# Kernel tuning notes

Measured on AMD Instinct MI355X. Metric: run time of the kernel, lower is better.

## Reference

```python
import math
import jax, jax.numpy as jnp
import numpy as np

B, L, D_MODEL = 2, 2048, 1024
N_HEAD, HEAD_DIM = 16, 64
ATT_SCALE = 1.0  # divisor is sqrt(head_dim ** attention_scale)


def setup_inputs() -> dict:
    key = jax.random.key(0)
    ks = jax.random.split(key, 6)
    HD = N_HEAD * HEAD_DIM
    # Xavier-uniform style init for projection weights (stored as [in, out])
    def xavier(k, fan_in, fan_out):
        lim = math.sqrt(6.0 / (fan_in + fan_out))
        return jax.random.uniform(k, (fan_in, fan_out), jnp.float32, -lim, lim)
    return {
        "x":  jax.random.normal(ks[0], (B, L, D_MODEL), jnp.float32),
        "Wq": xavier(ks[1], D_MODEL, HD), "bq": jnp.zeros((HD,), jnp.float32),
        "Wk": xavier(ks[2], D_MODEL, HD), "bk": jnp.zeros((HD,), jnp.float32),
        "Wv": xavier(ks[3], D_MODEL, HD), "bv": jnp.zeros((HD,), jnp.float32),
        "Wo": xavier(ks[4], HD, D_MODEL),
        "bo": jax.random.uniform(ks[5], (D_MODEL,), jnp.float32, -1.0 / math.sqrt(HD), 1.0 / math.sqrt(HD)),
    }


def reference(x, Wq, bq, Wk, bk, Wv, bv, Wo, bo):
    b, l, _ = x.shape
    # QKV projections -> [B, L, H, Dh]
    q = (x @ Wq + bq).reshape(b, l, N_HEAD, HEAD_DIM)
    k = (x @ Wk + bk).reshape(b, l, N_HEAD, HEAD_DIM)
    v = (x @ Wv + bv).reshape(b, l, N_HEAD, HEAD_DIM)
    scale = 1.0 / math.sqrt(HEAD_DIM ** ATT_SCALE)
    # Unnormalized (no softmax) attention: (Q K^T / sqrt(Dh)) V
    scores = jnp.einsum("blhd,bmhd->bhlm", q, k) * scale  # [B,H,L,L]
    attn = jnp.einsum("bhlm,bmhd->blhd", scores, v)        # [B,L,H,Dh]
    out = attn.reshape(b, l, N_HEAD * HEAD_DIM) @ Wo + bo  # dispatcher
    return out
```

## Files before the change

kernel.cpp:

```cpp
#include <hip/hip_runtime.h>
#include <stdint.h>

#define B_ 2
#define L_ 2048
#define DM 1024
#define NH 16
#define DH 64
#define M_ (B_*L_)
#define NQKV 3072

typedef short short8 __attribute__((ext_vector_type(8)));
typedef float f32x4 __attribute__((ext_vector_type(4)));

__device__ __forceinline__ unsigned short f2b(float f) {
    union { float f; unsigned int u; } v; v.f = f;
    unsigned int u = v.u;
    return (unsigned short)((u + 0x7fffu + ((u >> 16) & 1u)) >> 16);
}

__device__ __forceinline__ void gld_lds16(const void* g, void* l) {
    __builtin_amdgcn_global_load_lds(
        (const __attribute__((address_space(1))) void*)g,
        (__attribute__((address_space(3))) void*)l, 16, 0, 0);
}

__global__ __launch_bounds__(256)
void setup_kernel(const float* __restrict__ x,
                  const float* __restrict__ Wq, const float* __restrict__ Wk,
                  const float* __restrict__ Wv, const float* __restrict__ Wo,
                  const float* __restrict__ bq, const float* __restrict__ bk,
                  const float* __restrict__ bv,
                  unsigned short* __restrict__ xb, unsigned short* __restrict__ WqkvT,
                  unsigned short* __restrict__ WoT, float* __restrict__ biasq,
                  float* __restrict__ KtV)
{
    __shared__ float tile[32][33];
    const int bid = blockIdx.x;
    const int t = threadIdx.x;

    if (bid < 2048) {
        int i = (bid * 256 + t) * 8;
        float4 a0 = *(const float4*)(x + i);
        float4 a1 = *(const float4*)(x + i + 4);
        uint4 p;
        p.x = (unsigned)f2b(a0.x) | ((unsigned)f2b(a0.y) << 16);
        p.y = (unsigned)f2b(a0.z) | ((unsigned)f2b(a0.w) << 16);
        p.z = (unsigned)f2b(a1.x) | ((unsigned)f2b(a1.y) << 16);
        p.w = (unsigned)f2b(a1.z) | ((unsigned)f2b(a1.w) << 16);
        *(uint4*)(xb + i) = p;
    } else if (bid < 2048 + 4096) {
        int wb = bid - 2048;
        int wi = wb >> 10;
        int tid = wb & 1023;
        const float* W = (wi == 0) ? Wq : (wi == 1) ? Wk : (wi == 2) ? Wv : Wo;
        float s = (wi == 1) ? 0.125f : 1.0f;
        int n0 = (tid & 31) * 32, k0 = (tid >> 5) * 32;
        int r = t >> 3, c4 = (t & 7) << 2;
        float4 v = *(const float4*)(W + (size_t)(k0 + r) * DM + n0 + c4);
        tile[r][c4+0] = v.x; tile[r][c4+1] = v.y; tile[r][c4+2] = v.z; tile[r][c4+3] = v.w;
        __syncthreads();
        uint2 o;
        o.x = (unsigned)f2b(tile[c4+0][r]*s) | ((unsigned)f2b(tile[c4+1][r]*s) << 16);
        o.y = (unsigned)f2b(tile[c4+2][r]*s) | ((unsigned)f2b(tile[c4+3][r]*s) << 16);
        int f = n0 + r;
        size_t drow;
        unsigned short* dst;
        if (wi == 0)      { dst = WqkvT; drow = f; }
        else if (wi == 1) { dst = WqkvT; drow = 1024 + (f >> 6) * 128 + (f & 63); }
        else if (wi == 2) { dst = WqkvT; drow = 1024 + (f >> 6) * 128 + 64 + (f & 63); }
        else              { dst = WoT;   drow = f; }
        *(uint2*)(dst + drow * DM + k0 + c4) = o;
    } else if (bid < 2048 + 4096 + 12) {
        int n = (bid - 6144) * 256 + t;
        float v;
        if (n < 1024) v = bq[n];
        else {
            int kv = (n - 1024) >> 7, r = (n - 1024) & 127;
            v = (r < 64) ? 0.125f * bk[kv * 64 + r] : bv[kv * 64 + (r - 64)];
        }
        biasq[n] = v;
    } else {
        int i = ((bid - 6156) * 256 + t) * 4;
        float4 z; z.x = z.y = z.z = z.w = 0.f;
        *(float4*)(KtV + i) = z;
    }
}

__global__ __launch_bounds__(256)
void qkv_fused_kernel(const unsigned short* __restrict__ A,
                      const unsigned short* __restrict__ Bt,
                      const float* __restrict__ biasq,
                      unsigned short* __restrict__ Qb,
                      float* __restrict__ KtV)
{
    __shared__ __align__(16) char smem[34816];
    unsigned short* As = (unsigned short*)smem;
    unsigned short* Bs = (unsigned short*)(smem + 8192);

    const int bid = blockIdx.x;
    const int xcd = bid & 7, local = bid >> 3;
    const int mt = xcd * 4 + (local & 3);
    const int nt = local >> 2;
    const int m0 = mt * 128, n0 = nt * 128;

    const int t = threadIdx.x;
    const int w = t >> 6, lane = t & 63;
    const int quad = lane >> 4, l16 = lane & 15;
    const int wm = w >> 1, wn = w & 1;

    f32x4 acc[4][4];
    #pragma unroll
    for (int i = 0; i < 4; i++)
        #pragma unroll
        for (int j = 0; j < 4; j++)
            #pragma unroll
            for (int r = 0; r < 4; r++) acc[i][j][r] = 0.f;

    const int srow = t >> 2;
    const int schunk = t & 3;

    for (int kk = 0; kk < DM; kk += 32) {
        #pragma unroll
        for (int p = 0; p < 2; p++) {
            int row = p * 64 + srow;
            int g = schunk ^ ((row >> 1) & 3);
            gld_lds16(A  + (size_t)(m0 + row) * DM + kk + g * 8,
                      (char*)As + p * 4096 + w * 1024);
            gld_lds16(Bt + (size_t)(n0 + row) * DM + kk + g * 8,
                      (char*)Bs + p * 4096 + w * 1024);
        }
        __syncthreads();

        short8 afr[4], bfr[4];
        #pragma unroll
        for (int i = 0; i < 4; i++) {
            int am = wm * 64 + i * 16 + l16;
            afr[i] = *(const short8*)((const char*)As + am * 64 + ((quad ^ ((am >> 1) & 3)) << 4));
            int bn = wn * 64 + i * 16 + l16;
            bfr[i] = *(const short8*)((const char*)Bs + bn * 64 + ((quad ^ ((bn >> 1) & 3)) << 4));
        }
        #pragma unroll
        for (int i = 0; i < 4; i++)
            #pragma unroll
            for (int j = 0; j < 4; j++)
                acc[i][j] = __builtin_amdgcn_mfma_f32_16x16x32_bf16(afr[i], bfr[j], acc[i][j], 0, 0, 0);
        __syncthreads();
    }

    #pragma unroll
    for (int j = 0; j < 4; j++) {
        float bv = biasq[n0 + wn * 64 + j * 16 + l16];
        #pragma unroll
        for (int i = 0; i < 4; i++)
            #pragma unroll
            for (int r = 0; r < 4; r++) acc[i][j][r] += bv;
    }

    if (nt < 8) {
        #pragma unroll
        for (int j = 0; j < 4; j++) {
            int col = n0 + wn * 64 + j * 16 + l16;
            #pragma unroll
            for (int i = 0; i < 4; i++) {
                #pragma unroll
                for (int r = 0; r < 4; r++) {
                    int row = m0 + wm * 64 + i * 16 + quad * 4 + r;
                    Qb[(size_t)row * DM + col] = f2b(acc[i][j][r]);
                }
            }
        }
        return;
    }

    const int h  = nt - 8;
    const int bh = (m0 >> 11) * NH + h;
    unsigned short (*Xt)[136] = (unsigned short (*)[136])smem;

    #pragma unroll
    for (int j = 0; j < 4; j++) {
        int c = wn * 64 + j * 16 + l16;
        #pragma unroll
        for (int i = 0; i < 4; i++) {
            int l0 = wm * 64 + i * 16 + quad * 4;
            uint2 o;
            o.x = (unsigned)f2b(acc[i][j][0]) | ((unsigned)f2b(acc[i][j][1]) << 16);
            o.y = (unsigned)f2b(acc[i][j][2]) | ((unsigned)f2b(acc[i][j][3]) << 16);
            *(uint2*)&Xt[c][l0] = o;
        }
    }
    __syncthreads();

    f32x4 kacc[4];
    #pragma unroll
    for (int j = 0; j < 4; j++)
        #pragma unroll
        for (int r = 0; r < 4; r++) kacc[j][r] = 0.f;

    #pragma unroll
    for (int ks = 0; ks < 4; ks++) {
        short8 af = *(const short8*)&Xt[w * 16 + l16][ks * 32 + quad * 8];
        #pragma unroll
        for (int j = 0; j < 4; j++) {
            short8 bfr = *(const short8*)&Xt[64 + j * 16 + l16][ks * 32 + quad * 8];
            kacc[j] = __builtin_amdgcn_mfma_f32_16x16x32_bf16(af, bfr, kacc[j], 0, 0, 0);
        }
    }

    float* dst = KtV + (size_t)bh * 64 * 64;
    #pragma unroll
    for (int j = 0; j < 4; j++) {
        int col = j * 16 + l16;
        #pragma unroll
        for (int r = 0; r < 4; r++) {
            int row = w * 16 + quad * 4 + r;
            atomicAdd(dst + row * 64 + col, kacc[j][r]);
        }
    }
}

__global__ __launch_bounds__(256)
void zmat_kernel(const unsigned short* __restrict__ WoT, const float* __restrict__ KtV,
                 unsigned short* __restrict__ ZT)
{
    __shared__ __align__(16) unsigned short Asl[64][72];
    __shared__ __align__(16) unsigned short Bsl[64][72];

    const int bh = blockIdx.x, nt0 = blockIdx.y;
    const int b = bh >> 4, h = bh & 15;
    const int t = threadIdx.x;
    const int wave = t >> 6, lane = t & 63;
    const int quad = lane >> 4, l16 = lane & 15;
    const int n0 = nt0 * 64;
    const int row = t >> 2, c0 = (t & 3) << 4;

    const unsigned short* ap = WoT + (size_t)(n0 + row) * DM + h * DH + c0;
    *(uint4*)&Asl[row][c0]     = *(const uint4*)ap;
    *(uint4*)&Asl[row][c0 + 8] = *(const uint4*)(ap + 8);

    const float* kp = KtV + ((size_t)bh * 64 + row) * 64 + c0;
    #pragma unroll
    for (int j = 0; j < 16; j++) Bsl[row][c0 + j] = f2b(kp[j]);
    __syncthreads();

    f32x4 acc[4];
    #pragma unroll
    for (int i = 0; i < 4; i++)
        #pragma unroll
        for (int r = 0; r < 4; r++) acc[i][r] = 0.f;

    #pragma unroll
    for (int ks = 0; ks < 2; ks++) {
        short8 af = *(const short8*)&Asl[wave * 16 + l16][ks * 32 + quad * 8];
        #pragma unroll
        for (int nt = 0; nt < 4; nt++) {
            short8 bfr = *(const short8*)&Bsl[nt * 16 + l16][ks * 32 + quad * 8];
            acc[nt] = __builtin_amdgcn_mfma_f32_16x16x32_bf16(af, bfr, acc[nt], 0, 0, 0);
        }
    }

    unsigned short* zb = ZT + (size_t)b * 1024 * 1024 + (size_t)h * DH;
    #pragma unroll
    for (int nt = 0; nt < 4; nt++) {
        int col = nt * 16 + l16;
        #pragma unroll
        for (int r = 0; r < 4; r++) {
            int zr = n0 + wave * 16 + quad * 4 + r;
            zb[(size_t)zr * 1024 + col] = f2b(acc[nt][r]);
        }
    }
}

__global__ __launch_bounds__(256)
void out_gemm_kernel(const unsigned short* __restrict__ A,
                     const unsigned short* __restrict__ Bt,
                     const float* __restrict__ bias,
                     float* __restrict__ C)
{
    __shared__ __align__(16) unsigned short As[128 * 64];
    __shared__ __align__(16) unsigned short Bs[64 * 64];

    const int bid = blockIdx.x;
    const int xcd = bid & 7, local = bid >> 3;
    const int mt = xcd * 4 + (local & 3);
    const int nt = local >> 2;
    const int m0 = mt * 128, n0 = nt * 64;

    const int t = threadIdx.x;
    const int w = t >> 6, lane = t & 63;
    const int quad = lane >> 4, l16 = lane & 15;

    const unsigned short* Btb = Bt + (size_t)(m0 >> 11) * 1024 * 1024;

    f32x4 acc[2][4];
    #pragma unroll
    for (int i = 0; i < 2; i++)
        #pragma unroll
        for (int j = 0; j < 4; j++)
            #pragma unroll
            for (int r = 0; r < 4; r++) acc[i][j][r] = 0.f;

    for (int kk = 0; kk < DM; kk += 64) {
        #pragma unroll
        for (int p = 0; p < 4; p++) {
            int c = p * 256 + t;
            int row = c >> 3, slot = c & 7;
            int g = slot ^ ((row >> 1) & 7);
            gld_lds16(A + (size_t)(m0 + row) * DM + kk + g * 8,
                      (char*)As + p * 4096 + w * 1024);
        }
        #pragma unroll
        for (int p = 0; p < 2; p++) {
            int c = p * 256 + t;
            int row = c >> 3, slot = c & 7;
            int g = slot ^ ((row >> 1) & 7);
            gld_lds16(Btb + (size_t)(n0 + row) * DM + kk + g * 8,
                      (char*)Bs + p * 4096 + w * 1024);
        }
        __syncthreads();

        #pragma unroll
        for (int ks = 0; ks < 2; ks++) {
            int kc = ks * 4 + quad;
            short8 afr[2], bfr[4];
            #pragma unroll
            for (int i = 0; i < 2; i++) {
                int am = w * 32 + i * 16 + l16;
                afr[i] = *(const short8*)((const char*)As + am * 128 + ((kc ^ ((am >> 1) & 7)) << 4));
            }
            #pragma unroll
            for (int j = 0; j < 4; j++) {
                int bn = j * 16 + l16;
                bfr[j] = *(const short8*)((const char*)Bs + bn * 128 + ((kc ^ ((bn >> 1) & 7)) << 4));
            }
            #pragma unroll
            for (int i = 0; i < 2; i++)
                #pragma unroll
                for (int j = 0; j < 4; j++)
                    acc[i][j] = __builtin_amdgcn_mfma_f32_16x16x32_bf16(afr[i], bfr[j], acc[i][j], 0, 0, 0);
        }
        __syncthreads();
    }

    #pragma unroll
    for (int j = 0; j < 4; j++) {
        int col = n0 + j * 16 + l16;
        float bv = bias[col];
        #pragma unroll
        for (int i = 0; i < 2; i++) {
            #pragma unroll
            for (int r = 0; r < 4; r++) {
                int row = m0 + w * 32 + i * 16 + quad * 4 + r;
                C[(size_t)row * DM + col] = acc[i][j][r] + bv;
            }
        }
    }
}


extern "C" void kernel_launch(void* const* d_in, const int* in_sizes, int n_in,
                              void* d_out, int out_size, void* d_ws, size_t ws_size,
                              hipStream_t stream)
{
    const float* x  = (const float*)d_in[0];
    const float* Wq = (const float*)d_in[1];
    const float* bq = (const float*)d_in[2];
    const float* Wk = (const float*)d_in[3];
    const float* bk = (const float*)d_in[4];
    const float* Wv = (const float*)d_in[5];
    const float* bv = (const float*)d_in[6];
    const float* Wo = (const float*)d_in[7];
    const float* bo = (const float*)d_in[8];

    char* ws = (char*)d_ws;
    unsigned short* xb    = (unsigned short*)(ws);
    unsigned short* WqkvT = (unsigned short*)(ws + (size_t)8  * 1024 * 1024);
    unsigned short* WoT   = (unsigned short*)(ws + (size_t)14 * 1024 * 1024);
    float*          biasq = (float*)         (ws + (size_t)16 * 1024 * 1024);
    unsigned short* Qb    = (unsigned short*)(ws + (size_t)17 * 1024 * 1024);
    unsigned short* ZT    = (unsigned short*)(ws + (size_t)25 * 1024 * 1024);
    float*          KtV   = (float*)         (ws + (size_t)29 * 1024 * 1024);

    setup_kernel<<<6284, 256, 0, stream>>>(x, Wq, Wk, Wv, Wo, bq, bk, bv,
                                           xb, WqkvT, WoT, biasq, KtV);

    qkv_fused_kernel<<<768, 256, 0, stream>>>(xb, WqkvT, biasq, Qb, KtV);

    zmat_kernel<<<dim3(B_ * NH, 16), 256, 0, stream>>>(WoT, KtV, ZT);

    out_gemm_kernel<<<512, 256, 0, stream>>>(Qb, ZT, bo, (float*)d_out);
}
```

Baseline: 143.3 us.

## Fold Q projection and Wo into per-batch combined weight matrix

Instead of computing Q = xWq and then Q·Z, precompute per batch P = [Wq;bq]·KtV per head and M = Wo^T·P^T, so the output is x·M plus a bias row folded in via an augmented row. This removes the Q GEMM (a third of the QKV projection) and the Qb write/read, replacing it with two smaller weight-sized GEMMs per batch. It adds an extra kernel launch and an extra bf16 rounding of the combined matrix, which changes numerics slightly.

Result: slower. 155.1 us (+8.2%).

```diff
diff --git a/kernel.cpp b/kernel.cpp
--- a/kernel.cpp
+++ b/kernel.cpp
@@ -7,7 +7,7 @@
 #define NH 16
 #define DH 64
 #define M_ (B_*L_)
-#define NQKV 3072
+#define KP 1152
 
 typedef short short8 __attribute__((ext_vector_type(8)));
 typedef float f32x4 __attribute__((ext_vector_type(4)));
@@ -16,6 +16,11 @@
     union { float f; unsigned int u; } v; v.f = f;
     unsigned int u = v.u;
     return (unsigned short)((u + 0x7fffu + ((u >> 16) & 1u)) >> 16);
+}
+
+__device__ __forceinline__ float b2f(unsigned short b) {
+    union { float f; unsigned int u; } v; v.u = ((unsigned)b) << 16;
+    return v.f;
 }
 
 __device__ __forceinline__ void gld_lds16(const void* g, void* l) {
@@ -30,9 +35,9 @@
                   const float* __restrict__ Wv, const float* __restrict__ Wo,
                   const float* __restrict__ bq, const float* __restrict__ bk,
                   const float* __restrict__ bv,
-                  unsigned short* __restrict__ xb, unsigned short* __restrict__ WqkvT,
-                  unsigned short* __restrict__ WoT, float* __restrict__ biasq,
-                  float* __restrict__ KtV)
+                  unsigned short* __restrict__ xb, unsigned short* __restrict__ WkvT,
+                  unsigned short* __restrict__ WoT, unsigned short* __restrict__ WqA,
+                  float* __restrict__ biaskv, float* __restrict__ KtV)
 {
     __shared__ float tile[32][33];
     const int bid = blockIdx.x;
@@ -48,12 +53,12 @@
         p.z = (unsigned)f2b(a1.x) | ((unsigned)f2b(a1.y) << 16);
         p.w = (unsigned)f2b(a1.z) | ((unsigned)f2b(a1.w) << 16);
         *(uint4*)(xb + i) = p;
-    } else if (bid < 2048 + 4096) {
+    } else if (bid < 2048 + 3072) {
         int wb = bid - 2048;
         int wi = wb >> 10;
         int tid = wb & 1023;
-        const float* W = (wi == 0) ? Wq : (wi == 1) ? Wk : (wi == 2) ? Wv : Wo;
-        float s = (wi == 1) ? 0.125f : 1.0f;
+        const float* W = (wi == 0) ? Wk : (wi == 1) ? Wv : Wo;
+        float s = (wi == 0) ? 0.125f : 1.0f;
         int n0 = (tid & 31) * 32, k0 = (tid >> 5) * 32;
         int r = t >> 3, c4 = (t & 7) << 2;
         float4 v = *(const float4*)(W + (size_t)(k0 + r) * DM + n0 + c4);
@@ -65,33 +70,66 @@
         int f = n0 + r;
         size_t drow;
         unsigned short* dst;
-        if (wi == 0)      { dst = WqkvT; drow = f; }
-        else if (wi == 1) { dst = WqkvT; drow = 1024 + (f >> 6) * 128 + (f & 63); }
-        else if (wi == 2) { dst = WqkvT; drow = 1024 + (f >> 6) * 128 + 64 + (f & 63); }
-        else              { dst = WoT;   drow = f; }
+        if (wi == 0)      { dst = WkvT; drow = (f >> 6) * 128 + (f & 63); }
+        else if (wi == 1) { dst = WkvT; drow = (f >> 6) * 128 + 64 + (f & 63); }
+        else              { dst = WoT;  drow = f; }
         *(uint2*)(dst + drow * DM + k0 + c4) = o;
-    } else if (bid < 2048 + 4096 + 12) {
-        int n = (bid - 6144) * 256 + t;
-        float v;
-        if (n < 1024) v = bq[n];
-        else {
-            int kv = (n - 1024) >> 7, r = (n - 1024) & 127;
-            v = (r < 64) ? 0.125f * bk[kv * 64 + r] : bv[kv * 64 + (r - 64)];
-        }
-        biasq[n] = v;
+    } else if (bid < 2048 + 3072 + 512) {
+        int i = ((bid - 5120) * 256 + t) * 8;
+        float4 a0 = *(const float4*)(Wq + i);
+        float4 a1 = *(const float4*)(Wq + i + 4);
+        uint4 p;
+        p.x = (unsigned)f2b(a0.x) | ((unsigned)f2b(a0.y) << 16);
+        p.y = (unsigned)f2b(a0.z) | ((unsigned)f2b(a0.w) << 16);
+        p.z = (unsigned)f2b(a1.x) | ((unsigned)f2b(a1.y) << 16);
+        p.w = (unsigned)f2b(a1.z) | ((unsigned)f2b(a1.w) << 16);
+        *(uint4*)(WqA + i) = p;
+    } else if (bid < 2048 + 3072 + 512 + 64) {
+        int idx = ((bid - 5632) * 256 + t) * 8;
+        uint4 p;
+        if (idx < 1024) {
+            float4 a0 = *(const float4*)(bq + idx);
+            float4 a1 = *(const float4*)(bq + idx + 4);
+            p.x = (unsigned)f2b(a0.x) | ((unsigned)f2b(a0.y) << 16);
+            p.y = (unsigned)f2b(a0.z) | ((unsigned)f2b(a0.w) << 16);
+            p.z = (unsigned)f2b(a1.x) | ((unsigned)f2b(a1.y) << 16);
+            p.w = (unsigned)f2b(a1.z) | ((unsigned)f2b(a1.w) << 16);
+        } else {
+            p.x = p.y = p.z = p.w = 0u;
+        }
+        *(uint4*)(WqA + 1024 * 1024 + idx) = p;
+    } else if (bid < 2048 + 3072 + 512 + 64 + 2) {
+        int i = ((bid - 5696) * 256 + t) * 4;
+        float o0, o1, o2, o3;
+        {
+            int n = i + 0, kv = n >> 7, rr = n & 127;
+            o0 = (rr < 64) ? 0.125f * bk[kv * 64 + rr] : bv[kv * 64 + (rr - 64)];
+        }
+        {
+            int n = i + 1, kv = n >> 7, rr = n & 127;
+            o1 = (rr < 64) ? 0.125f * bk[kv * 64 + rr] : bv[kv * 64 + (rr - 64)];
+        }
+        {
+            int n = i + 2, kv = n >> 7, rr = n & 127;
+            o2 = (rr < 64) ? 0.125f * bk[kv * 64 + rr] : bv[kv * 64 + (rr - 64)];
+        }
+        {
+            int n = i + 3, kv = n >> 7, rr = n & 127;
+            o3 = (rr < 64) ? 0.125f * bk[kv * 64 + rr] : bv[kv * 64 + (rr - 64)];
+        }
+        *(float4*)(biaskv + i) = make_float4(o0, o1, o2, o3);
     } else {
-        int i = ((bid - 6156) * 256 + t) * 4;
+        int i = ((bid - 5698) * 256 + t) * 4;
         float4 z; z.x = z.y = z.z = z.w = 0.f;
         *(float4*)(KtV + i) = z;
     }
 }
 
 __global__ __launch_bounds__(256)
-void qkv_fused_kernel(const unsigned short* __restrict__ A,
-                      const unsigned short* __restrict__ Bt,
-                      const float* __restrict__ biasq,
-                      unsigned short* __restrict__ Qb,
-                      float* __restrict__ KtV)
+void kv_fused_kernel(const unsigned short* __restrict__ A,
+                     const unsigned short* __restrict__ Bt,
+                     const float* __restrict__ biaskv,
+                     float* __restrict__ KtV)
 {
     __shared__ __align__(16) char smem[34816];
     unsigned short* As = (unsigned short*)smem;
@@ -149,30 +187,14 @@
 
     #pragma unroll
     for (int j = 0; j < 4; j++) {
-        float bv = biasq[n0 + wn * 64 + j * 16 + l16];
+        float bvv = biaskv[n0 + wn * 64 + j * 16 + l16];
         #pragma unroll
         for (int i = 0; i < 4; i++)
             #pragma unroll
-            for (int r = 0; r < 4; r++) acc[i][j][r] += bv;
-    }
-
-    if (nt < 8) {
-        #pragma unroll
-        for (int j = 0; j < 4; j++) {
-            int col = n0 + wn * 64 + j * 16 + l16;
-            #pragma unroll
-            for (int i = 0; i < 4; i++) {
-                #pragma unroll
-                for (int r = 0; r < 4; r++) {
-                    int row = m0 + wm * 64 + i * 16 + quad * 4 + r;
-                    Qb[(size_t)row * DM + col] = f2b(acc[i][j][r]);
-                }
-            }
-        }
-        return;
-    }
-
-    const int h  = nt - 8;
+            for (int r = 0; r < 4; r++) acc[i][j][r] += bvv;
+    }
+
+    const int h  = nt;
     const int bh = (m0 >> 11) * NH + h;
     unsigned short (*Xt)[136] = (unsigned short (*)[136])smem;
 
@@ -219,54 +241,155 @@
 }
 
 __global__ __launch_bounds__(256)
-void zmat_kernel(const unsigned short* __restrict__ WoT, const float* __restrict__ KtV,
-                 unsigned short* __restrict__ ZT)
+void pmat_kernel(const unsigned short* __restrict__ WqA, const float* __restrict__ KtV,
+                 unsigned short* __restrict__ P)
 {
-    __shared__ __align__(16) unsigned short Asl[64][72];
-    __shared__ __align__(16) unsigned short Bsl[64][72];
-
-    const int bh = blockIdx.x, nt0 = blockIdx.y;
+    __shared__ __align__(16) unsigned short As[128 * 64];
+    __shared__ __align__(16) unsigned short Bs[64][72];
+
+    const int bh = blockIdx.x;
+    const int rt = blockIdx.y;
     const int b = bh >> 4, h = bh & 15;
     const int t = threadIdx.x;
-    const int wave = t >> 6, lane = t & 63;
+    const int w = t >> 6, lane = t & 63;
     const int quad = lane >> 4, l16 = lane & 15;
-    const int n0 = nt0 * 64;
-    const int row = t >> 2, c0 = (t & 3) << 4;
-
-    const unsigned short* ap = WoT + (size_t)(n0 + row) * DM + h * DH + c0;
-    *(uint4*)&Asl[row][c0]     = *(const uint4*)ap;
-    *(uint4*)&Asl[row][c0 + 8] = *(const uint4*)(ap + 8);
-
-    const float* kp = KtV + ((size_t)bh * 64 + row) * 64 + c0;
-    #pragma unroll
-    for (int j = 0; j < 16; j++) Bsl[row][c0 + j] = f2b(kp[j]);
+
+    #pragma unroll
+    for (int p = 0; p < 4; p++) {
+        int c = p * 256 + t;
+        int row = c >> 3, slot = c & 7;
+        int g = slot ^ ((row >> 1) & 7);
+        gld_lds16(WqA + (size_t)(rt * 128 + row) * DM + h * 64 + g * 8,
+                  (char*)As + p * 4096 + w * 1024);
+    }
+    {
+        const int d1 = t >> 2, c0 = (t & 3) * 16;
+        const float* kp = KtV + (size_t)bh * 64 * 64 + d1 * 64 + c0;
+        #pragma unroll
+        for (int j = 0; j < 16; j++)
+            Bs[c0 + j][d1] = f2b(kp[j]);
+    }
     __syncthreads();
 
-    f32x4 acc[4];
-    #pragma unroll
-    for (int i = 0; i < 4; i++)
-        #pragma unroll
-        for (int r = 0; r < 4; r++) acc[i][r] = 0.f;
+    f32x4 acc[2][4];
+    #pragma unroll
+    for (int i = 0; i < 2; i++)
+        #pragma unroll
+        for (int j = 0; j < 4; j++)
+            #pragma unroll
+            for (int r = 0; r < 4; r++) acc[i][j][r] = 0.f;
 
     #pragma unroll
     for (int ks = 0; ks < 2; ks++) {
-        short8 af = *(const short8*)&Asl[wave * 16 + l16][ks * 32 + quad * 8];
-        #pragma unroll
-        for (int nt = 0; nt < 4; nt++) {
-            short8 bfr = *(const short8*)&Bsl[nt * 16 + l16][ks * 32 + quad * 8];
-            acc[nt] = __builtin_amdgcn_mfma_f32_16x16x32_bf16(af, bfr, acc[nt], 0, 0, 0);
-        }
-    }
-
-    unsigned short* zb = ZT + (size_t)b * 1024 * 1024 + (size_t)h * DH;
-    #pragma unroll
-    for (int nt = 0; nt < 4; nt++) {
-        int col = nt * 16 + l16;
-        #pragma unroll
-        for (int r = 0; r < 4; r++) {
-            int zr = n0 + wave * 16 + quad * 4 + r;
-            zb[(size_t)zr * 1024 + col] = f2b(acc[nt][r]);
-        }
+        int kc = ks * 4 + quad;
+        short8 afr[2], bfr[4];
+        #pragma unroll
+        for (int i = 0; i < 2; i++) {
+            int am = w * 32 + i * 16 + l16;
+            afr[i] = *(const short8*)((const char*)As + am * 128 + ((kc ^ ((am >> 1) & 7)) << 4));
+        }
+        #pragma unroll
+        for (int j = 0; j < 4; j++)
+            bfr[j] = *(const short8*)&Bs[j * 16 + l16][ks * 32 + quad * 8];
+        #pragma unroll
+        for (int i = 0; i < 2; i++)
+            #pragma unroll
+            for (int j = 0; j < 4; j++)
+                acc[i][j] = __builtin_amdgcn_mfma_f32_16x16x32_bf16(afr[i], bfr[j], acc[i][j], 0, 0, 0);
+    }
+
+    unsigned short* pb = P + ((size_t)b * KP + rt * 128) * DM + h * 64;
+    #pragma unroll
+    for (int j = 0; j < 4; j++) {
+        int col = j * 16 + l16;
+        #pragma unroll
+        for (int i = 0; i < 2; i++)
+            #pragma unroll
+            for (int rr = 0; rr < 4; rr++) {
+                int row = w * 32 + i * 16 + quad * 4 + rr;
+                pb[(size_t)row * DM + col] = f2b(acc[i][j][rr]);
+            }
+    }
+}
+
+__global__ __launch_bounds__(256)
+void mmat_kernel(const unsigned short* __restrict__ WoT, const unsigned short* __restrict__ P,
+                 unsigned short* __restrict__ MT)
+{
+    __shared__ __align__(16) unsigned short As[128 * 64];
+    __shared__ __align__(16) unsigned short Bs[64 * 64];
+
+    const int bid = blockIdx.x;
+    const int bb = bid / 144;
+    const int r144 = bid % 144;
+    const int mt = r144 & 7, nt = r144 >> 3;
+    const int m0 = mt * 128, n0 = nt * 64;
+
+    const int t = threadIdx.x;
+    const int w = t >> 6, lane = t & 63;
+    const int quad = lane >> 4, l16 = lane & 15;
+
+    f32x4 acc[2][4];
+    #pragma unroll
+    for (int i = 0; i < 2; i++)
+        #pragma unroll
+        for (int j = 0; j < 4; j++)
+            #pragma unroll
+            for (int r = 0; r < 4; r++) acc[i][j][r] = 0.f;
+
+    for (int kk = 0; kk < DM; kk += 64) {
+        #pragma unroll
+        for (int p = 0; p < 4; p++) {
+            int c = p * 256 + t;
+            int row = c >> 3, slot = c & 7;
+            int g = slot ^ ((row >> 1) & 7);
+            gld_lds16(WoT + (size_t)(m0 + row) * DM + kk + g * 8,
+                      (char*)As + p * 4096 + w * 1024);
+        }
+        #pragma unroll
+        for (int p = 0; p < 2; p++) {
+            int c = p * 256 + t;
+            int row = c >> 3, slot = c & 7;
+            int g = slot ^ ((row >> 1) & 7);
+            gld_lds16(P + ((size_t)bb * KP + n0 + row) * DM + kk + g * 8,
+                      (char*)Bs + p * 4096 + w * 1024);
+        }
+        __syncthreads();
+
+        #pragma unroll
+        for (int ks = 0; ks < 2; ks++) {
+            int kc = ks * 4 + quad;
+            short8 afr[2], bfr[4];
+            #pragma unroll
+            for (int i = 0; i < 2; i++) {
+                int am = w * 32 + i * 16 + l16;
+                afr[i] = *(const short8*)((const char*)As + am * 128 + ((kc ^ ((am >> 1) & 7)) << 4));
+            }
+            #pragma unroll
+            for (int j = 0; j < 4; j++) {
+                int bn = j * 16 + l16;
+                bfr[j] = *(const short8*)((const char*)Bs + bn * 128 + ((kc ^ ((bn >> 1) & 7)) << 4));
+            }
+            #pragma unroll
+            for (int i = 0; i < 2; i++)
+                #pragma unroll
+                for (int j = 0; j < 4; j++)
+                    acc[i][j] = __builtin_amdgcn_mfma_f32_16x16x32_bf16(afr[i], bfr[j], acc[i][j], 0, 0, 0);
+        }
+        __syncthreads();
+    }
+
+    unsigned short* mb = MT + (size_t)bb * 1024 * KP;
+    #pragma unroll
+    for (int j = 0; j < 4; j++) {
+        int col = n0 + j * 16 + l16;
+        #pragma unroll
+        for (int i = 0; i < 2; i++)
+            #pragma unroll
+            for (int rr = 0; rr < 4; rr++) {
+                int row = m0 + w * 32 + i * 16 + quad * 4 + rr;
+                mb[(size_t)row * KP + col] = f2b(acc[i][j][rr]);
+            }
     }
 }
 
@@ -289,7 +412,7 @@
     const int w = t >> 6, lane = t & 63;
     const int quad = lane >> 4, l16 = lane & 15;
 
-    const unsigned short* Btb = Bt + (size_t)(m0 >> 11) * 1024 * 1024;
+    const unsigned short* Btb = Bt + (size_t)(m0 >> 11) * 1024 * KP;
 
     f32x4 acc[2][4];
     #pragma unroll
@@ -313,7 +436,7 @@
             int c = p * 256 + t;
             int row = c >> 3, slot = c & 7;
             int g = slot ^ ((row >> 1) & 7);
-            gld_lds16(Btb + (size_t)(n0 + row) * DM + kk + g * 8,
+            gld_lds16(Btb + (size_t)(n0 + row) * KP + kk + g * 8,
                       (char*)Bs + p * 4096 + w * 1024);
         }
         __syncthreads();
@@ -344,13 +467,13 @@
     #pragma unroll
     for (int j = 0; j < 4; j++) {
         int col = n0 + j * 16 + l16;
-        float bv = bias[col];
+        float bvv = bias[col] + b2f(Btb[(size_t)col * KP + 1024]);
         #pragma unroll
         for (int i = 0; i < 2; i++) {
             #pragma unroll
             for (int r = 0; r < 4; r++) {
                 int row = m0 + w * 32 + i * 16 + quad * 4 + r;
-                C[(size_t)row * DM + col] = acc[i][j][r] + bv;
+                C[(size_t)row * DM + col] = acc[i][j][r] + bvv;
             }
         }
     }
@@ -372,20 +495,23 @@
     const float* bo = (const float*)d_in[8];
 
     char* ws = (char*)d_ws;
-    unsigned short* xb    = (unsigned short*)(ws);
-    unsigned short* WqkvT = (unsigned short*)(ws + (size_t)8  * 1024 * 1024);
-    unsigned short* WoT   = (unsigned short*)(ws + (size_t)14 * 1024 * 1024);
-    float*          biasq = (float*)         (ws + (size_t)16 * 1024 * 1024);
-    unsigned short* Qb    = (unsigned short*)(ws + (size_t)17 * 1024 * 1024);
-    unsigned short* ZT    = (unsigned short*)(ws + (size_t)25 * 1024 * 1024);
-    float*          KtV   = (float*)         (ws + (size_t)29 * 1024 * 1024);
-
-    setup_kernel<<<6284, 256, 0, stream>>>(x, Wq, Wk, Wv, Wo, bq, bk, bv,
-                                           xb, WqkvT, WoT, biasq, KtV);
-
-    qkv_fused_kernel<<<768, 256, 0, stream>>>(xb, WqkvT, biasq, Qb, KtV);
-
-    zmat_kernel<<<dim3(B_ * NH, 16), 256, 0, stream>>>(WoT, KtV, ZT);
-
-    out_gemm_kernel<<<512, 256, 0, stream>>>(Qb, ZT, bo, (float*)d_out);
-}
+    unsigned short* xb     = (unsigned short*)(ws);
+    unsigned short* WkvT   = (unsigned short*)(ws + (size_t)8  * 1024 * 1024);
+    unsigned short* WoT    = (unsigned short*)(ws + (size_t)12 * 1024 * 1024);
+    unsigned short* WqA    = (unsigned short*)(ws + (size_t)14 * 1024 * 1024);
+    float*          biaskv = (float*)         (ws + (size_t)16 * 1024 * 1024 + 262144);
+    float*          KtV    = (float*)         (ws + (size_t)17 * 1024 * 1024);
+    unsigned short* P      = (unsigned short*)(ws + (size_t)18 * 1024 * 1024);
+    unsigned short* MT     = (unsigned short*)(ws + (size_t)23 * 1024 * 1024);
+
+    setup_kernel<<<5826, 256, 0, stream>>>(x, Wq, Wk, Wv, Wo, bq, bk, bv,
+                                           xb, WkvT, WoT, WqA, biaskv, KtV);
+
+    kv_fused_kernel<<<512, 256, 0, stream>>>(xb, WkvT, biaskv, KtV);
+
+    pmat_kernel<<<dim3(32, 9), 256, 0, stream>>>(WqA, KtV, P);
+
+    mmat_kernel<<<288, 256, 0, stream>>>(WoT, P, MT);
+
+    out_gemm_kernel<<<512, 256, 0, stream>>>(xb, MT, bo, (float*)d_out);
+}
```

## Deepen QKV GEMM K-step to 64 and enlarge output GEMM tile to 128x128

Applied to the files above, without the earlier changes.

The QKV GEMM now stages a 64-wide K slice per iteration instead of 32, using an 8-chunk XOR swizzle and two MFMA sub-steps per barrier pair. This halves the number of synchronisation rounds. The output GEMM moves from 128x64 to 128x128 tiles with a 2x2 wave layout and 16 accumulators per wave, which halves the grid to 256 blocks. The larger tiles improve data reuse per LDS load, at the cost of more LDS and registers per block and fewer blocks to fill the CUs.

Measured after the change: 158.2 us. +10.4%, slower.

```diff
diff --git a/kernel.cpp b/kernel.cpp
--- a/kernel.cpp
+++ b/kernel.cpp
@@ -95,7 +95,7 @@
 {
     __shared__ __align__(16) char smem[34816];
     unsigned short* As = (unsigned short*)smem;
-    unsigned short* Bs = (unsigned short*)(smem + 8192);
+    unsigned short* Bs = (unsigned short*)(smem + 16384);
 
     const int bid = blockIdx.x;
     const int xcd = bid & 7, local = bid >> 3;
@@ -116,34 +116,42 @@
             #pragma unroll
             for (int r = 0; r < 4; r++) acc[i][j][r] = 0.f;
 
-    const int srow = t >> 2;
-    const int schunk = t & 3;
-
-    for (int kk = 0; kk < DM; kk += 32) {
-        #pragma unroll
-        for (int p = 0; p < 2; p++) {
-            int row = p * 64 + srow;
-            int g = schunk ^ ((row >> 1) & 3);
-            gld_lds16(A  + (size_t)(m0 + row) * DM + kk + g * 8,
+    for (int kk = 0; kk < DM; kk += 64) {
+        #pragma unroll
+        for (int p = 0; p < 4; p++) {
+            int c = p * 256 + t;
+            int row = c >> 3, slot = c & 7;
+            int g = slot ^ ((row >> 1) & 7);
+            gld_lds16(A + (size_t)(m0 + row) * DM + kk + g * 8,
                       (char*)As + p * 4096 + w * 1024);
+        }
+        #pragma unroll
+        for (int p = 0; p < 4; p++) {
+            int c = p * 256 + t;
+            int row = c >> 3, slot = c & 7;
+            int g = slot ^ ((row >> 1) & 7);
             gld_lds16(Bt + (size_t)(n0 + row) * DM + kk + g * 8,
                       (char*)Bs + p * 4096 + w * 1024);
         }
         __syncthreads();
 
-        short8 afr[4], bfr[4];
-        #pragma unroll
-        for (int i = 0; i < 4; i++) {
-            int am = wm * 64 + i * 16 + l16;
-            afr[i] = *(const short8*)((const char*)As + am * 64 + ((quad ^ ((am >> 1) & 3)) << 4));
-            int bn = wn * 64 + i * 16 + l16;
-            bfr[i] = *(const short8*)((const char*)Bs + bn * 64 + ((quad ^ ((bn >> 1) & 3)) << 4));
-        }
-        #pragma unroll
-        for (int i = 0; i < 4; i++)
-            #pragma unroll
-            for (int j = 0; j < 4; j++)
-                acc[i][j] = __builtin_amdgcn_mfma_f32_16x16x32_bf16(afr[i], bfr[j], acc[i][j], 0, 0, 0);
+        #pragma unroll
+        for (int ks = 0; ks < 2; ks++) {
+            int kc = ks * 4 + quad;
+            short8 afr[4], bfr[4];
+            #pragma unroll
+            for (int i = 0; i < 4; i++) {
+                int am = wm * 64 + i * 16 + l16;
+                afr[i] = *(const short8*)((const char*)As + am * 128 + ((kc ^ ((am >> 1) & 7)) << 4));
+                int bn = wn * 64 + i * 16 + l16;
+                bfr[i] = *(const short8*)((const char*)Bs + bn * 128 + ((kc ^ ((bn >> 1) & 7)) << 4));
+            }
+            #pragma unroll
+            for (int i = 0; i < 4; i++)
+                #pragma unroll
+                for (int j = 0; j < 4; j++)
+                    acc[i][j] = __builtin_amdgcn_mfma_f32_16x16x32_bf16(afr[i], bfr[j], acc[i][j], 0, 0, 0);
+        }
         __syncthreads();
     }
 
@@ -277,23 +285,24 @@
                      float* __restrict__ C)
 {
     __shared__ __align__(16) unsigned short As[128 * 64];
-    __shared__ __align__(16) unsigned short Bs[64 * 64];
+    __shared__ __align__(16) unsigned short Bs[128 * 64];
 
     const int bid = blockIdx.x;
     const int xcd = bid & 7, local = bid >> 3;
     const int mt = xcd * 4 + (local & 3);
     const int nt = local >> 2;
-    const int m0 = mt * 128, n0 = nt * 64;
+    const int m0 = mt * 128, n0 = nt * 128;
 
     const int t = threadIdx.x;
     const int w = t >> 6, lane = t & 63;
     const int quad = lane >> 4, l16 = lane & 15;
+    const int wm = w >> 1, wn = w & 1;
 
     const unsigned short* Btb = Bt + (size_t)(m0 >> 11) * 1024 * 1024;
 
-    f32x4 acc[2][4];
-    #pragma unroll
-    for (int i = 0; i < 2; i++)
+    f32x4 acc[4][4];
+    #pragma unroll
+    for (int i = 0; i < 4; i++)
         #pragma unroll
         for (int j = 0; j < 4; j++)
             #pragma unroll
@@ -309,7 +318,7 @@
                       (char*)As + p * 4096 + w * 1024);
         }
         #pragma unroll
-        for (int p = 0; p < 2; p++) {
+        for (int p = 0; p < 4; p++) {
             int c = p * 256 + t;
             int row = c >> 3, slot = c & 7;
             int g = slot ^ ((row >> 1) & 7);
@@ -321,19 +330,16 @@
         #pragma unroll
         for (int ks = 0; ks < 2; ks++) {
             int kc = ks * 4 + quad;
-            short8 afr[2], bfr[4];
-            #pragma unroll
-            for (int i = 0; i < 2; i++) {
-                int am = w * 32 + i * 16 + l16;
+            short8 afr[4], bfr[4];
+            #pragma unroll
+            for (int i = 0; i < 4; i++) {
+                int am = wm * 64 + i * 16 + l16;
                 afr[i] = *(const short8*)((const char*)As + am * 128 + ((kc ^ ((am >> 1) & 7)) << 4));
+                int bn = wn * 64 + i * 16 + l16;
+                bfr[i] = *(const short8*)((const char*)Bs + bn * 128 + ((kc ^ ((bn >> 1) & 7)) << 4));
             }
             #pragma unroll
-            for (int j = 0; j < 4; j++) {
-                int bn = j * 16 + l16;
-                bfr[j] = *(const short8*)((const char*)Bs + bn * 128 + ((kc ^ ((bn >> 1) & 7)) << 4));
-            }
-            #pragma unroll
-            for (int i = 0; i < 2; i++)
+            for (int i = 0; i < 4; i++)
                 #pragma unroll
                 for (int j = 0; j < 4; j++)
                     acc[i][j] = __builtin_amdgcn_mfma_f32_16x16x32_bf16(afr[i], bfr[j], acc[i][j], 0, 0, 0);
@@ -343,13 +349,13 @@
 
     #pragma unroll
     for (int j = 0; j < 4; j++) {
-        int col = n0 + j * 16 + l16;
+        int col = n0 + wn * 64 + j * 16 + l16;
         float bv = bias[col];
         #pragma unroll
-        for (int i = 0; i < 2; i++) {
+        for (int i = 0; i < 4; i++) {
             #pragma unroll
             for (int r = 0; r < 4; r++) {
-                int row = m0 + w * 32 + i * 16 + quad * 4 + r;
+                int row = m0 + wm * 64 + i * 16 + quad * 4 + r;
                 C[(size_t)row * DM + col] = acc[i][j][r] + bv;
             }
         }
@@ -387,5 +393,5 @@
 
     zmat_kernel<<<dim3(B_ * NH, 16), 256, 0, stream>>>(WoT, KtV, ZT);
 
-    out_gemm_kernel<<<512, 256, 0, stream>>>(Qb, ZT, bo, (float*)d_out);
-}
+    out_gemm_kernel<<<256, 256, 0, stream>>>(Qb, ZT, bo, (float*)d_out);
+}
```

## Double-buffer LDS tiles in QKV and output GEMM main loops

Applied to the files above, without the earlier changes.

Both the fused QKV GEMM and the output projection GEMM now use two LDS buffers. The next k-tile's global-to-LDS loads are issued before the MFMA work on the current tile, leaving one barrier per iteration instead of two. The aim is to hide global load latency behind compute. The output GEMM's LDS footprint grows to 48KB, and an extra barrier is added before the QKV epilogue reuses shared memory, both of which may reduce occupancy.

Measured after the change: 150.6 us. 1.05x slower.

```diff
diff --git a/kernel.cpp b/kernel.cpp
--- a/kernel.cpp
+++ b/kernel.cpp
@@ -94,8 +94,6 @@
                       float* __restrict__ KtV)
 {
     __shared__ __align__(16) char smem[34816];
-    unsigned short* As = (unsigned short*)smem;
-    unsigned short* Bs = (unsigned short*)(smem + 8192);
 
     const int bid = blockIdx.x;
     const int xcd = bid & 7, local = bid >> 3;
@@ -119,33 +117,45 @@
     const int srow = t >> 2;
     const int schunk = t & 3;
 
-    for (int kk = 0; kk < DM; kk += 32) {
+    auto stage = [&](int buf, int kk) {
         #pragma unroll
         for (int p = 0; p < 2; p++) {
             int row = p * 64 + srow;
             int g = schunk ^ ((row >> 1) & 3);
             gld_lds16(A  + (size_t)(m0 + row) * DM + kk + g * 8,
-                      (char*)As + p * 4096 + w * 1024);
+                      smem + buf * 16384 + p * 4096 + w * 1024);
             gld_lds16(Bt + (size_t)(n0 + row) * DM + kk + g * 8,
-                      (char*)Bs + p * 4096 + w * 1024);
-        }
-        __syncthreads();
-
+                      smem + buf * 16384 + 8192 + p * 4096 + w * 1024);
+        }
+    };
+    auto compute = [&](int buf) {
+        const char* Asb = smem + buf * 16384;
+        const char* Bsb = Asb + 8192;
         short8 afr[4], bfr[4];
         #pragma unroll
         for (int i = 0; i < 4; i++) {
             int am = wm * 64 + i * 16 + l16;
-            afr[i] = *(const short8*)((const char*)As + am * 64 + ((quad ^ ((am >> 1) & 3)) << 4));
+            afr[i] = *(const short8*)(Asb + am * 64 + ((quad ^ ((am >> 1) & 3)) << 4));
             int bn = wn * 64 + i * 16 + l16;
-            bfr[i] = *(const short8*)((const char*)Bs + bn * 64 + ((quad ^ ((bn >> 1) & 3)) << 4));
+            bfr[i] = *(const short8*)(Bsb + bn * 64 + ((quad ^ ((bn >> 1) & 3)) << 4));
         }
         #pragma unroll
         for (int i = 0; i < 4; i++)
             #pragma unroll
             for (int j = 0; j < 4; j++)
                 acc[i][j] = __builtin_amdgcn_mfma_f32_16x16x32_bf16(afr[i], bfr[j], acc[i][j], 0, 0, 0);
+    };
+
+    stage(0, 0);
+    __syncthreads();
+    int cur = 0;
+    for (int kk = 0; kk < DM - 32; kk += 32) {
+        stage(cur ^ 1, kk + 32);
+        compute(cur);
         __syncthreads();
-    }
+        cur ^= 1;
+    }
+    compute(cur);
 
     #pragma unroll
     for (int j = 0; j < 4; j++) {
@@ -176,6 +186,8 @@
     const int bh = (m0 >> 11) * NH + h;
     unsigned short (*Xt)[136] = (unsigned short (*)[136])smem;
 
+    __syncthreads();
+
     #pragma unroll
     for (int j = 0; j < 4; j++) {
         int c = wn * 64 + j * 16 + l16;
@@ -276,8 +288,7 @@
                      const float* __restrict__ bias,
                      float* __restrict__ C)
 {
-    __shared__ __align__(16) unsigned short As[128 * 64];
-    __shared__ __align__(16) unsigned short Bs[64 * 64];
+    __shared__ __align__(16) char smem[49152];
 
     const int bid = blockIdx.x;
     const int xcd = bid & 7, local = bid >> 3;
@@ -299,14 +310,14 @@
             #pragma unroll
             for (int r = 0; r < 4; r++) acc[i][j][r] = 0.f;
 
-    for (int kk = 0; kk < DM; kk += 64) {
+    auto stage = [&](int buf, int kk) {
         #pragma unroll
         for (int p = 0; p < 4; p++) {
             int c = p * 256 + t;
             int row = c >> 3, slot = c & 7;
             int g = slot ^ ((row >> 1) & 7);
             gld_lds16(A + (size_t)(m0 + row) * DM + kk + g * 8,
-                      (char*)As + p * 4096 + w * 1024);
+                      smem + buf * 24576 + p * 4096 + w * 1024);
         }
         #pragma unroll
         for (int p = 0; p < 2; p++) {
@@ -314,10 +325,12 @@
             int row = c >> 3, slot = c & 7;
             int g = slot ^ ((row >> 1) & 7);
             gld_lds16(Btb + (size_t)(n0 + row) * DM + kk + g * 8,
-                      (char*)Bs + p * 4096 + w * 1024);
-        }
-        __syncthreads();
-
+                      smem + buf * 24576 + 16384 + p * 4096 + w * 1024);
+        }
+    };
+    auto compute = [&](int buf) {
+        const char* Asb = smem + buf * 24576;
+        const char* Bsb = Asb + 16384;
         #pragma unroll
         for (int ks = 0; ks < 2; ks++) {
             int kc = ks * 4 + quad;
@@ -325,12 +338,12 @@
             #pragma unroll
             for (int i = 0; i < 2; i++) {
                 int am = w * 32 + i * 16 + l16;
-                afr[i] = *(const short8*)((const char*)As + am * 128 + ((kc ^ ((am >> 1) & 7)) << 4));
+                afr[i] = *(const short8*)(Asb + am * 128 + ((kc ^ ((am >> 1) & 7)) << 4));
             }
             #pragma unroll
             for (int j = 0; j < 4; j++) {
                 int bn = j * 16 + l16;
-                bfr[j] = *(const short8*)((const char*)Bs + bn * 128 + ((kc ^ ((bn >> 1) & 7)) << 4));
+                bfr[j] = *(const short8*)(Bsb + bn * 128 + ((kc ^ ((bn >> 1) & 7)) << 4));
             }
             #pragma unroll
             for (int i = 0; i < 2; i++)
@@ -338,8 +351,18 @@
                 for (int j = 0; j < 4; j++)
                     acc[i][j] = __builtin_amdgcn_mfma_f32_16x16x32_bf16(afr[i], bfr[j], acc[i][j], 0, 0, 0);
         }
+    };
+
+    stage(0, 0);
+    __syncthreads();
+    int cur = 0;
+    for (int kk = 0; kk < DM - 64; kk += 64) {
+        stage(cur ^ 1, kk + 64);
+        compute(cur);
         __syncthreads();
-    }
+        cur ^= 1;
+    }
+    compute(cur);
 
     #pragma unroll
     for (int j = 0; j < 4; j++) {
```
